# Kernel tuning notes

Hardware: AMD Instinct MI355X
Metric: run time of the kernel (lower is better)

## Reference

```python
import jax, jax.numpy as jnp
import numpy as np

N_ADDR, N_TX = 150000, 200000
IN_DIM, HID, HEADS = 64, 32, 4
DIM = HID // HEADS
E_AT, E_TA, E_AA = 1000000, 1000000, 500000
SLOPE = 0.2  # HANConv default negative_slope


def setup_inputs() -> dict:
    key = jax.random.key(0)
    ks = jax.random.split(key, 16)
    f = lambda k, shape, s: jax.random.normal(k, shape, dtype=jnp.float32) * s
    return {
        "x_addr": f(ks[0], (N_ADDR, IN_DIM), 1.0),
        "x_tx": f(ks[1], (N_TX, IN_DIM), 1.0),
        "e_at_src": jax.random.randint(ks[2], (E_AT,), 0, N_ADDR, dtype=jnp.int32),
        "e_at_dst": jax.random.randint(ks[3], (E_AT,), 0, N_TX, dtype=jnp.int32),
        "e_ta_src": jax.random.randint(ks[4], (E_TA,), 0, N_TX, dtype=jnp.int32),
        "e_ta_dst": jax.random.randint(ks[5], (E_TA,), 0, N_ADDR, dtype=jnp.int32),
        "e_aa_src": jax.random.randint(ks[6], (E_AA,), 0, N_ADDR, dtype=jnp.int32),
        "e_aa_dst": jax.random.randint(ks[7], (E_AA,), 0, N_ADDR, dtype=jnp.int32),
        "pW1": f(ks[8], (2, IN_DIM, HID), 0.1),      # layer-1 proj per node type [addr, tx]
        "pb1": jnp.zeros((2, HID), jnp.float32),
        "pW23": f(ks[9], (2, 2, HID, HID), 0.1),     # [layer-1, node_type]
        "pb23": jnp.zeros((2, 2, HID), jnp.float32),
        "att_src": f(ks[10], (3, 3, HEADS, DIM), 0.1),  # [layer, edge_type, H, D]
        "att_dst": f(ks[11], (3, 3, HEADS, DIM), 0.1),
        "kW": f(ks[12], (3, HID, HID), 0.1),         # semantic k_lin per layer
        "kb": jnp.zeros((3, HID), jnp.float32),
        "q": f(ks[13], (3, HID), 0.1),               # semantic query per layer
        "linW": f(ks[14], (HID, 2), 0.1),
        "linb": jnp.zeros((2,), jnp.float32),
    }


def _edge_softmax(logits, dst, n):
    # numerically stable segment softmax over destination neighborhoods
    m = jax.ops.segment_max(logits, dst, num_segments=n)          # [n, H]
    m = jnp.where(jnp.isfinite(m), m, 0.0)
    e = jnp.exp(logits - m[dst])
    s = jax.ops.segment_sum(e, dst, num_segments=n)
    return e / (s[dst] + 1e-16)


def _relation(h_src, h_dst, src, dst, a_s, a_d, n_dst):
    alpha_src = jnp.einsum('nhd,hd->nh', h_src, a_s)
    alpha_dst = jnp.einsum('nhd,hd->nh', h_dst, a_d)
    logit = alpha_src[src] + alpha_dst[dst]                        # [E, H]
    logit = jnp.where(logit >= 0, logit, SLOPE * logit)            # leaky_relu
    alpha = _edge_softmax(logit, dst, n_dst)
    msg = h_src[src] * alpha[:, :, None]                           # [E, H, D]
    out = jax.ops.segment_sum(msg, dst, num_segments=n_dst)        # [n_dst, H, D]
    return jax.nn.relu(out.reshape(n_dst, HID))


def _semantic(xs, kW, kb, q):
    # xs: [R, N, F]; semantic-level attention over R relations (PyG `group`)
    t = jnp.tanh(xs @ kW + kb).mean(axis=1)       # [R, F]
    attn = jax.nn.softmax((t * q).sum(-1))        # [R]
    return jnp.einsum('r,rnf->nf', attn, xs)


def _han_layer(x_a, x_t, Wa, ba, Wt, bt, a_s, a_d, kW, kb, q, edges):
    h_a = (x_a @ Wa + ba).reshape(-1, HEADS, DIM)
    h_t = (x_t @ Wt + bt).reshape(-1, HEADS, DIM)
    o_tx = _relation(h_a, h_t, edges[0], edges[1], a_s[0], a_d[0], N_TX)
    o_a1 = _relation(h_t, h_a, edges[2], edges[3], a_s[1], a_d[1], N_ADDR)
    o_a2 = _relation(h_a, h_a, edges[4], edges[5], a_s[2], a_d[2], N_ADDR)
    new_a = _semantic(jnp.stack([o_a1, o_a2]), kW, kb, q)
    new_t = _semantic(o_tx[None], kW, kb, q)
    return new_a, new_t


def reference(x_addr, x_tx, e_at_src, e_at_dst, e_ta_src, e_ta_dst,
              e_aa_src, e_aa_dst, pW1, pb1, pW23, pb23, att_src, att_dst,
              kW, kb, q, linW, linb):
    edges = (e_at_src, e_at_dst, e_ta_src, e_ta_dst, e_aa_src, e_aa_dst)
    a, t = _han_layer(x_addr, x_tx, pW1[0], pb1[0], pW1[1], pb1[1],
                      att_src[0], att_dst[0], kW[0], kb[0], q[0], edges)
    a, t = jax.nn.relu(a), jax.nn.relu(t)  # wrapper relu; dropout = eval identity
    for l in range(2):
        a, t = _han_layer(a, t, pW23[l, 0], pb23[l, 0], pW23[l, 1], pb23[l, 1],
                          att_src[l + 1], att_dst[l + 1],
                          kW[l + 1], kb[l + 1], q[l + 1], edges)
        a, t = jax.nn.relu(a), jax.nn.relu(t)
    return a @ linW + linb
```

## Files before the change

### kernel.cpp

```cpp
#include <hip/hip_runtime.h>
#include <hip/hip_bf16.h>
#include <hip/hip_fp16.h>

#define NA 150000
#define NT 200000
#define E_AT 1000000
#define E_TA 1000000
#define E_AA 500000

#define CHK 4096
#define CAP 8192
#define P_AT 391
#define P_TA 293
#define P_AA 293
#define NBINS (P_AT + P_TA + P_AA)
#define CB_AT 245
#define CB_TA 245
#define CB_AA 123
#define NBBIN (CB_AT + CB_TA + CB_AA)

#define GB_AT 6250
#define GB_TA 4688
#define GB_AA 4688

// ... 47 lines not shown
                       float* __restrict__ wts, int* __restrict__ flagp,
                       int* __restrict__ gcnt, float* __restrict__ sem) {
    __shared__ int cnt;
    const int t = threadIdx.x;
    if (t == 0) cnt = 0;
    __syncthreads();
    const unsigned short* u = (const unsigned short*)x;
    int wild = 0;
    for (int i = t; i < 4096; i += 256) {
        unsigned short v = u[i];
        int e = (v >> 7) & 0xFF;
        if (e > 133 || (e != 0 && e < 100)) wild++;
        else if (e == 0 && (v & 0x7F)) wild++;
    }
    atomicAdd(&cnt, wild);
    __syncthreads();
    const int f32 = (cnt > 1024) ? 1 : 0;
    if (t == 0) *flagp = f32;
    if (t < 8) sem[t] = 0.f;
    for (int i = t; i < 1024; i += 256) gcnt[i] = 0;
    for (int i = t; i < 4096; i += 256) wts[WO_W1 + i]  = ldf(pW1, i, f32);
    for (int i = t; i < 64;   i += 256) wts[WO_B1 + i]  = ldf(pb1, i, f32);
    for (int i = t; i < 4096; i += 256) wts[WO_W23 + i] = ldf(pW23, i, f32);
    for (int i = t; i < 128;  i += 256) wts[WO_B23 + i] = ldf(pb23, i, f32);
    for (int i = t; i < 288;  i += 256) wts[WO_AS + i]  = ldf(attS, i, f32);
    for (int i = t; i < 288;  i += 256) wts[WO_AD + i]  = ldf(attD, i, f32);
    for (int i = t; i < 3072; i += 256) wts[WO_KW + i]  = ldf(kW, i, f32);
    for (int i = t; i < 96;   i += 256) wts[WO_KB + i]  = ldf(kb, i, f32);
    for (int i = t; i < 96;   i += 256) wts[WO_Q + i]   = ldf(qv, i, f32);
    for (int i = t; i < 64;   i += 256) wts[WO_LW + i]  = ldf(linW, i, f32);
    for (int i = t; i < 2;    i += 256) wts[WO_LB + i]  = ldf(linb, i, f32);
}

__global__ __launch_bounds__(256) void k_projbin(
        const void* __restrict__ Xa, const void* __restrict__ Xt,
        const float* __restrict__ W, const float* __restrict__ Bv,
        unsigned short* __restrict__ Ha, unsigned short* __restrict__ Ht,
        const float* __restrict__ attD,
        float* __restrict__ ad0, float* __restrict__ ad1, float* __restrict__ ad2,
        const int* __restrict__ flagp,
        const int* __restrict__ eat_s, const int* __restrict__ eat_d,
        const int* __restrict__ eta_s, const int* __restrict__ eta_d,
        const int* __restrict__ eaa_s, const int* __restrict__ eaa_d,
        int* __restrict__ gcnt,
        int* __restrict__ slot_at, int* __restrict__ slot_ta, int* __restrict__ slot_aa) {
    __shared__ float smem[4224];
    const int t = threadIdx.x;
    int b = blockIdx.x;
    if (b < NBBIN) {
        int* hist = (int*)smem;
        const int *src, *dst; int E, P, seg; int* slot;
        if (b < CB_AT)              { src = eat_s; dst = eat_d; E = E_AT; P = P_AT; seg = 0;            slot = slot_at; }
        else if (b < CB_AT + CB_TA) { b -= CB_AT;  src = eta_s; dst = eta_d; E = E_TA; P = P_TA; seg = P_AT;        slot = slot_ta; }
        else                        { b -= CB_AT + CB_TA; src = eaa_s; dst = eaa_d; E = E_AA; P = P_AA; seg = P_AT + P_TA; slot = slot_aa; }
        long e0 = (long)b * CHK;
        for (int i = t; i < P; i += 256) hist[i] = 0;
        __syncthreads();
        for (int k = 0; k < CHK; k += 256) {
            long e = e0 + k + t;
            if (e < E) atomicAdd(&hist[dst[e] >> 9], 1);
        }
        __syncthreads();
        for (int i = t; i < P; i += 256) {
            int v = hist[i];
            hist[i] = atomicAdd(&gcnt[seg + i], v);
        }
        __syncthreads();
        for (int k = 0; k < CHK; k += 256) {
            long e = e0 + k + t;
            if (e < E) {
                int d = dst[e];
                int bin = d >> 9;
                int pos = atomicAdd(&hist[bin], 1);
                slot[bin * CAP + pos] = ((d & 511) << 18) | src[e];
            }
        }
        return;
    }
    b -= NBBIN;
    constexpr int K = 64, XS = K + 4, CPR = K / 4, TOT4 = 32 * CPR;
    float* Xs = smem;
    float* Wl = smem + 2176;
    const bool isA = b < GA32;
    const int bb = isA ? b : b - GA32;
    const int N = isA ? NA : NT;
    const int wOff = isA ? 0 : 2048;
    const int bOff = isA ? 0 : 32;
    const long n0 = (long)bb * 32;
    for (int i = t; i < K * 32; i += 256) Wl[i] = W[wOff + i];
    {
        const void* X = isA ? Xa : Xt;
        const int f32 = *flagp;
        if (f32) {
            const float* Xf = (const float*)X;
            for (int i = t; i < TOT4; i += 256) {
                int r = i / CPR, c = (i & (CPR - 1)) * 4;
                long gr = n0 + r; if (gr >= N) gr = N - 1;
                *(float4*)&Xs[r * XS + c] = *(const float4*)&Xf[gr * K + c];
            }
        } else {
            const unsigned short* Xh = (const unsigned short*)X;
            for (int i = t; i < TOT4; i += 256) {
                int r = i / CPR, c = (i & (CPR - 1)) * 4;
                long gr = n0 + r; if (gr >= N) gr = N - 1;
                ushort4 v = *(const ushort4*)&Xh[gr * K + c];
                float4 o;
                o.x = bf2f(v.x); o.y = bf2f(v.y); o.z = bf2f(v.z); o.w = bf2f(v.w);
                *(float4*)&Xs[r * XS + c] = o;
            }
        }
    }
    __syncthreads();
    const int g = t >> 3, q = t & 7;
    const long n = n0 + g;
    float a0 = Bv[bOff + q * 4 + 0];
    float a1 = Bv[bOff + q * 4 + 1];
    float a2 = Bv[bOff + q * 4 + 2];
    float a3 = Bv[bOff + q * 4 + 3];
#pragma unroll 4
    for (int k4 = 0; k4 < K; k4 += 4) {
        float4 xv = *(const float4*)&Xs[g * XS + k4];
        float4 w0 = *(const float4*)&Wl[(k4 + 0) * 32 + q * 4];
        float4 w1 = *(const float4*)&Wl[(k4 + 1) * 32 + q * 4];
        float4 w2 = *(const float4*)&Wl[(k4 + 2) * 32 + q * 4];
        float4 w3 = *(const float4*)&Wl[(k4 + 3) * 32 + q * 4];
        a0 = fmaf(xv.x, w0.x, a0); a1 = fmaf(xv.x, w0.y, a1);
        a2 = fmaf(xv.x, w0.z, a2); a3 = fmaf(xv.x, w0.w, a3);
        a0 = fmaf(xv.y, w1.x, a0); a1 = fmaf(xv.y, w1.y, a1);
        a2 = fmaf(xv.y, w1.z, a2); a3 = fmaf(xv.y, w1.w, a3);
        a0 = fmaf(xv.z, w2.x, a0); a1 = fmaf(xv.z, w2.y, a1);
        a2 = fmaf(xv.z, w2.z, a2); a3 = fmaf(xv.z, w2.w, a3);
        a0 = fmaf(xv.w, w3.x, a0); a1 = fmaf(xv.w, w3.y, a1);
        a2 = fmaf(xv.w, w3.z, a2); a3 = fmaf(xv.w, w3.w, a3);
    }
    if (n < N) {
        unsigned short* Hh = isA ? Ha : Ht;
        unsigned int p01 = (unsigned)f2h(a0) | ((unsigned)f2h(a1) << 16);
        unsigned int p23 = (unsigned)f2h(a2) | ((unsigned)f2h(a3) << 16);
        *(uint2*)&Hh[n * 32 + q * 4] = make_uint2(p01, p23);
        const int hh = q >> 1;
        const int ai = q * 4;
        if (isA) {
            float p1 = a0 * attD[ai + 32] + a1 * attD[ai + 33]
                     + a2 * attD[ai + 34] + a3 * attD[ai + 35];
            float p2 = a0 * attD[ai + 64] + a1 * attD[ai + 65]
                     + a2 * attD[ai + 66] + a3 * attD[ai + 67];
            float s1 = p1 + __shfl_xor(p1, 1);
            float s2 = p2 + __shfl_xor(p2, 1);
            if (!(q & 1)) { ad1[n * 4 + hh] = s1; ad2[n * 4 + hh] = s2; }
        } else {
            float p0 = a0 * attD[ai] + a1 * attD[ai + 1]
                     + a2 * attD[ai + 2] + a3 * attD[ai + 3];
            float s0 = p0 + __shfl_xor(p0, 1);
            if (!(q & 1)) ad0[n * 4 + hh] = s0;
        }
    }
}

__global__ __launch_bounds__(256) void k_proj2(
        const float* __restrict__ O1, const float* __restrict__ Ot,
        const float* __restrict__ O2, const float* __restrict__ semL,
        const float* __restrict__ W, int wOffA, int wOffT,
        const float* __restrict__ Bv, int bOffA, int bOffT,
        unsigned short* __restrict__ Ha, unsigned short* __restrict__ Ht,
        const float* __restrict__ attD, int lBase,
        float* __restrict__ ad0, float* __restrict__ ad1, float* __restrict__ ad2) {
    constexpr int K = 32, XS = K + 4, CPR = K / 4, TOT4 = 64 * CPR;
    __shared__ float Xs[64 * XS];
    __shared__ float Wl[K * 32];
    const int t = threadIdx.x;
    const bool isA = blockIdx.x < GA64;
    const int bb = isA ? (int)blockIdx.x : (int)blockIdx.x - GA64;
    const int N = isA ? NA : NT;
    const int wOff = isA ? wOffA : wOffT;
    const int bOff = isA ? bOffA : bOffT;
    const long n0 = (long)bb * 64;
    for (int i = t; i < K * 32; i += 256) Wl[i] = W[wOff + i];
    if (isA) {
        float s0 = semL[0] * (1.0f / NA), s1 = semL[1] * (1.0f / NA);
        float m = fmaxf(s0, s1);
        float e0 = __expf(s0 - m), e1 = __expf(s1 - m);
        float inv = 1.f / (e0 + e1);
        const float w0 = e0 * inv, w1 = e1 * inv;
        for (int i = t; i < TOT4; i += 256) {
            int r = i / CPR, c = (i & (CPR - 1)) * 4;
            long gr = n0 + r; if (gr >= N) gr = N - 1;
            float4 va = *(const float4*)&O1[gr * K + c];
            float4 vb = *(const float4*)&O2[gr * K + c];
            float4 o;
// ... 51 lines not shown
        if (isA) {
            float p1 = A0 * attD[ai + 32] + A1 * attD[ai + 33]
                     + A2 * attD[ai + 34] + A3 * attD[ai + 35];
            float p2 = A0 * attD[ai + 64] + A1 * attD[ai + 65]
                     + A2 * attD[ai + 66] + A3 * attD[ai + 67];
            float s1 = p1 + __shfl_xor(p1, 1);
            float s2 = p2 + __shfl_xor(p2, 1);
            if (!(q & 1)) { ad1[nA * 4 + hh] = s1; ad2[nA * 4 + hh] = s2; }
        } else {
            float p0 = A0 * attD[ai] + A1 * attD[ai + 1]
                     + A2 * attD[ai + 2] + A3 * attD[ai + 3];
            float s0 = p0 + __shfl_xor(p0, 1);
            if (!(q & 1)) ad0[nA * 4 + hh] = s0;
        }
    }
    if (nB < N) {
        unsigned int p01 = (unsigned)f2h(B0) | ((unsigned)f2h(B1) << 16);
        unsigned int p23 = (unsigned)f2h(B2) | ((unsigned)f2h(B3) << 16);
        *(uint2*)&Hh[nB * 32 + q * 4] = make_uint2(p01, p23);
        if (isA) {
            float p1 = B0 * attD[ai + 32] + B1 * attD[ai + 33]
                     + B2 * attD[ai + 34] + B3 * attD[ai + 35];
            float p2 = B0 * attD[ai + 64] + B1 * attD[ai + 65]
                     + B2 * attD[ai + 66] + B3 * attD[ai + 67];
            float s1 = p1 + __shfl_xor(p1, 1);
            float s2 = p2 + __shfl_xor(p2, 1);
            if (!(q & 1)) { ad1[nB * 4 + hh] = s1; ad2[nB * 4 + hh] = s2; }
        } else {
            float p0 = B0 * attD[ai] + B1 * attD[ai + 1]
                     + B2 * attD[ai + 2] + B3 * attD[ai + 3];
            float s0 = p0 + __shfl_xor(p0, 1);
            if (!(q & 1)) ad0[nB * 4 + hh] = s0;
        }
    }
}

__global__ __launch_bounds__(256) void k_binsort(
        const int* __restrict__ gcnt,
        const int* __restrict__ slot_at, const int* __restrict__ slot_ta,
        const int* __restrict__ slot_aa,
        int* __restrict__ off_at, int* __restrict__ off_ta, int* __restrict__ off_aa,
        int* __restrict__ csr_at, int* __restrict__ csr_ta, int* __restrict__ csr_aa) {
    __shared__ int sa[512], sb[512], cur[512];
    __shared__ int red[4];
    int b = blockIdx.x, t = threadIdx.x;
    const int* slot; int* off; int* csr; int N, bin, seg;
    if (b < P_AT)              { slot = slot_at; off = off_at; csr = csr_at; N = NT; bin = b;                seg = 0; }
    else if (b < P_AT + P_TA)  { slot = slot_ta; off = off_ta; csr = csr_ta; N = NA; bin = b - P_AT;         seg = P_AT; }
    else                       { slot = slot_aa; off = off_aa; csr = csr_aa; N = NA; bin = b - P_AT - P_TA;  seg = P_AT + P_TA; }
    if (b == 0 && t == 0) { off_at[NT] = E_AT; off_ta[NA] = E_TA; off_aa[NA] = E_AA; }
    int part = 0;
    for (int i = t; i < bin; i += 256) part += gcnt[seg + i];
    for (int o = 32; o > 0; o >>= 1) part += __shfl_xor(part, o, 64);
    if ((t & 63) == 0) red[t >> 6] = part;
    sa[t] = 0; sa[t + 256] = 0;
    __syncthreads();
    const int base = red[0] + red[1] + red[2] + red[3];
    const int cnt  = gcnt[seg + bin];
    const int* sp = &slot[bin * CAP];
    for (int i = t; i < cnt; i += 256) atomicAdd(&sa[sp[i] >> 18], 1);
    __syncthreads();
    int* in = sa; int* out = sb;
    for (int o = 1; o < 512; o <<= 1) {
        for (int i = t; i < 512; i += 256)
            out[i] = in[i] + (i >= o ? in[i - o] : 0);
        __syncthreads();
        int* tmp = in; in = out; out = tmp;
    }
    for (int i = t; i < 512; i += 256) {
        int excl = i ? in[i - 1] : 0;
        cur[i] = excl;
        int gd = bin * 512 + i;
        if (gd < N) off[gd] = base + excl;
    }
    __syncthreads();
    for (int i = t; i < cnt; i += 256) {
        int pk = sp[i];
        int pos = atomicAdd(&cur[pk >> 18], 1);
        csr[base + pos] = pk & 0x3FFFF;
    }
}

__global__ __launch_bounds__(256) void k_gather3(
        const int* __restrict__ off_at, const int* __restrict__ csr_at,
        const int* __restrict__ off_ta, const int* __restrict__ csr_ta,
        const int* __restrict__ off_aa, const int* __restrict__ csr_aa,
        const float* __restrict__ ad0, const float* __restrict__ ad1,
        const float* __restrict__ ad2,
        const unsigned short* __restrict__ h_a, const unsigned short* __restrict__ h_t,
        float* __restrict__ o_tx, float* __restrict__ o_a1, float* __restrict__ o_a2,
        const float* __restrict__ attS, int lBase, int gbAT) {
    int b = blockIdx.x;
    const int *off, *csr;
    const float *ad_;
    const unsigned short* Hs;
    float* O;
    int N, attOff;
    if (b < gbAT) {
        off = off_at; csr = csr_at; ad_ = ad0; Hs = h_a; O = o_tx; N = NT;
        attOff = lBase;
    } else if (b < gbAT + GB_TA) {
        b -= gbAT;
        off = off_ta; csr = csr_ta; ad_ = ad1; Hs = h_t; O = o_a1; N = NA;
        attOff = lBase + 32;
    } else {
        b -= gbAT + GB_TA;
        off = off_aa; csr = csr_aa; ad_ = ad2; Hs = h_a; O = o_a2; N = NA;
        attOff = lBase + 64;
    }
    const int t = threadIdx.x;
    const int q = t & 7;
    const int hh = q >> 1;
    const int n = b * 32 + (t >> 3);
    if (n >= N) return;
    const float4 aq = *(const float4*)&attS[attOff + q * 4];
    const float aq0 = aq.x, aq1 = aq.y, aq2 = aq.z, aq3 = aq.w;
    const float adv = ad_[n * 4 + hh];
    const int p0 = off[n], p1 = off[n + 1];
    float ax = 0.f, ay = 0.f, az = 0.f, aw = 0.f, se = 0.f;
    int p = p0;
    for (; p + 4 <= p1; p += 4) {
        int s0 = csr[p], s1 = csr[p + 1], s2 = csr[p + 2], s3 = csr[p + 3];
        ushort4 v0 = *(const ushort4*)&Hs[s0 * 32 + q * 4];
        ushort4 v1 = *(const ushort4*)&Hs[s1 * 32 + q * 4];
        ushort4 v2 = *(const ushort4*)&Hs[s2 * 32 + q * 4];
        ushort4 v3 = *(const ushort4*)&Hs[s3 * 32 + q * 4];
        float h00 = h2f(v0.x), h01 = h2f(v0.y), h02 = h2f(v0.z), h03 = h2f(v0.w);
        float h10 = h2f(v1.x), h11 = h2f(v1.y), h12 = h2f(v1.z), h13 = h2f(v1.w);
        float h20 = h2f(v2.x), h21 = h2f(v2.y), h22 = h2f(v2.z), h23 = h2f(v2.w);
        float h30 = h2f(v3.x), h31 = h2f(v3.y), h32 = h2f(v3.z), h33 = h2f(v3.w);
        float pt0 = h00 * aq0 + h01 * aq1 + h02 * aq2 + h03 * aq3;
        float pt1 = h10 * aq0 + h11 * aq1 + h12 * aq2 + h13 * aq3;
        float pt2 = h20 * aq0 + h21 * aq1 + h22 * aq2 + h23 * aq3;
        float pt3 = h30 * aq0 + h31 * aq1 + h32 * aq2 + h33 * aq3;
        float al0 = pt0 + __shfl_xor(pt0, 1);
        float al1 = pt1 + __shfl_xor(pt1, 1);
        float al2 = pt2 + __shfl_xor(pt2, 1);
        float al3 = pt3 + __shfl_xor(pt3, 1);
        float l0 = al0 + adv; l0 = fmaxf(l0, 0.2f * l0); float e0 = __expf(l0);
        float l1 = al1 + adv; l1 = fmaxf(l1, 0.2f * l1); float e1 = __expf(l1);
        float l2 = al2 + adv; l2 = fmaxf(l2, 0.2f * l2); float e2 = __expf(l2);
        float l3 = al3 + adv; l3 = fmaxf(l3, 0.2f * l3); float e3 = __expf(l3);
        se += e0 + e1 + e2 + e3;
        ax += e0 * h00 + e1 * h10 + e2 * h20 + e3 * h30;
        ay += e0 * h01 + e1 * h11 + e2 * h21 + e3 * h31;
        az += e0 * h02 + e1 * h12 + e2 * h22 + e3 * h32;
        aw += e0 * h03 + e1 * h13 + e2 * h23 + e3 * h33;
    }
    for (; p < p1; p++) {
        int s = csr[p];
        ushort4 v = *(const ushort4*)&Hs[s * 32 + q * 4];
        float h0 = h2f(v.x), h1 = h2f(v.y), h2 = h2f(v.z), h3 = h2f(v.w);
        float pt = h0 * aq0 + h1 * aq1 + h2 * aq2 + h3 * aq3;
        float al = pt + __shfl_xor(pt, 1);
        float l = al + adv; l = fmaxf(l, 0.2f * l);
        float e = __expf(l);
        se += e;
        ax += e * h0; ay += e * h1; az += e * h2; aw += e * h3;
    }
    const float inv = 1.f / (se + 1e-16f);
    float4 r;
    r.x = fmaxf(ax * inv, 0.f);
    r.y = fmaxf(ay * inv, 0.f);
    r.z = fmaxf(az * inv, 0.f);
    r.w = fmaxf(aw * inv, 0.f);
    *(float4*)&O[n * 32 + q * 4] = r;
}

__global__ __launch_bounds__(256) void k_sem_reduce(
        const float* __restrict__ O1, const float* __restrict__ O2,
        const float* __restrict__ kWl, const float* __restrict__ kbl,
        const float* __restrict__ qvl, float* __restrict__ semL) {
    __shared__ float w[1088];
    __shared__ float bacc;
    const int t = threadIdx.x;
    const int r = (blockIdx.x >= NB_SEM) ? 1 : 0;
    const float* O = r ? O2 : O1;
    for (int i = t; i < 1024; i += 256) w[i] = kWl[i];
    if (t < 32) w[1024 + t] = kbl[t];
    if (t >= 64 && t < 96) w[1056 + (t - 64)] = qvl[t - 64];
    if (t == 0) bacc = 0.f;
    __syncthreads();
    long n = (long)(blockIdx.x - r * NB_SEM) * 256 + t;
    float S = 0.f;
    if (n < NA) {
        float x[32];
#pragma unroll
        for (int k = 0; k < 32; k++) x[k] = O[n * 32 + k];
#pragma unroll
        for (int f = 0; f < 32; f++) {
            float acc = w[1024 + f];
#pragma unroll
            for (int k = 0; k < 32; k++) acc += x[k] * w[k * 32 + f];
            S += ftanh(acc) * w[1056 + f];
        }
    }
    for (int o = 32; o > 0; o >>= 1) S += __shfl_xor(S, o, 64);
    if ((t & 63) == 0) atomicAdd(&bacc, S);
    __syncthreads();
    if (t == 0) atomicAdd(&semL[r], bacc);
}

__global__ void k_combine_final(const float* __restrict__ o1, const float* __restrict__ o2,
                                const float* __restrict__ semL,
                                const float* __restrict__ linW, const float* __restrict__ linb,
                                void* __restrict__ out, int N, const int* __restrict__ flagp) {
    int n = blockIdx.x * blockDim.x + threadIdx.x;
    if (n >= N) return;
    int f32 = *flagp;
    float q0 = semL[0] * (1.0f / NA), q1 = semL[1] * (1.0f / NA);
    float m = fmaxf(q0, q1);
    float e0 = __expf(q0 - m), e1 = __expf(q1 - m);
    float ai = 1.f / (e0 + e1);
    float w0 = e0 * ai, w1 = e1 * ai;
    float s0 = linb[0], s1 = linb[1];
    const float* p1 = &o1[(long)n * 32];
// ... 39 lines not shown

    const size_t NA32 = (size_t)NA * 32, NT32 = (size_t)NT * 32;
    const size_t NA4 = (size_t)NA * 4, NT4 = (size_t)NT * 4;

    float* ws    = (float*)d_ws;
    float* h_aF  = ws;
    float* h_tF  = h_aF + NA32;
    float* o_a1  = h_tF + NT32;
    float* o_a2  = o_a1 + NA32;
    float* o_tx  = o_a2 + NA32;
    float* ad1   = o_tx + NT32;
    float* ad2   = ad1 + NA4;
    float* ad0   = ad2 + NA4;
    float* sem   = ad0 + NT4;
    int*   flagp = (int*)(sem + 8);
    int*   off_at = flagp + 16;
    int*   off_ta = off_at + (NT + 1);
    int*   off_aa = off_ta + (NA + 1);
    int*   csr_at = off_aa + (NA + 1);
    int*   csr_ta = csr_at + E_AT;
    int*   csr_aa = csr_ta + E_TA;
    int*   gcnt   = csr_aa + E_AA;
    int*   slot_at = gcnt + 1024;
    int*   slot_ta = slot_at + P_AT * CAP;
    int*   slot_aa = slot_ta + P_TA * CAP;
    float* wts    = (float*)(slot_aa + (size_t)P_AA * CAP);

    unsigned short* h_a = (unsigned short*)h_aF;
    unsigned short* h_t = (unsigned short*)h_tF;

    k_init<<<1, 256, 0, stream>>>(x_addr, pW1, pb1, pW23, pb23, attS, attD,
                                  kW, kb, qv, linW, linb, wts, flagp, gcnt, sem);

    k_projbin<<<NBBIN + GA32 + GT32, 256, 0, stream>>>(
        x_addr, x_tx, wts + WO_W1, wts + WO_B1, h_a, h_t, wts + WO_AD,
        ad0, ad1, ad2, flagp,
        eat_s, eat_d, eta_s, eta_d, eaa_s, eaa_d,
        gcnt, slot_at, slot_ta, slot_aa);
    k_binsort<<<NBINS, 256, 0, stream>>>(gcnt, slot_at, slot_ta, slot_aa,
                                         off_at, off_ta, off_aa, csr_at, csr_ta, csr_aa);

    for (int l = 0; l < 3; l++) {
        if (l > 0) {
            int wi = (l - 1) * 2;
            k_proj2<<<GA64 + GT64, 256, 0, stream>>>(
                o_a1, o_tx, o_a2, sem + 2 * (l - 1),
                wts + WO_W23, (wi + 0) * 1024, (wi + 1) * 1024,
                wts + WO_B23, (wi + 0) * 32, (wi + 1) * 32,
                h_a, h_t, wts + WO_AD, l * 96, ad0, ad1, ad2);
        }
        const int gbAT = (l < 2) ? GB_AT : 0;
        k_gather3<<<gbAT + GB_TA + GB_AA, 256, 0, stream>>>(
            off_at, csr_at, off_ta, csr_ta, off_aa, csr_aa,
            ad0, ad1, ad2, h_a, h_t, o_tx, o_a1, o_a2, wts + WO_AS, l * 96, gbAT);
        k_sem_reduce<<<2 * NB_SEM, 256, 0, stream>>>(
            o_a1, o_a2, wts + WO_KW + l * 1024, wts + WO_KB + l * 32,
            wts + WO_Q + l * 32, sem + 2 * l);
        if (l == 2) {
            k_combine_final<<<gblocks(NA), 256, 0, stream>>>(o_a1, o_a2, sem + 4,
                                                             wts + WO_LW, wts + WO_LB,
                                                             d_out, NA, flagp);
        }
    }
}
```

Measured before the change: 543.2 us.

## Rebalance kernel fusion to overlap tx projection with bin sort and AT gather with semantic reduce

Splits the combined projection/binning kernel so the tx-node projection runs alongside the CSR bin sort in one launch, and the address projection runs with edge binning. In each layer, the address-side gathers run first, and the tx-side gather is fused with the semantic-attention reduction, which depends only on the address outputs. The goal is to fill idle GPU capacity in small or tail-heavy kernels with independent work. The cost is heterogeneous blocks sharing one launch's resource limits, which may hurt occupancy or scheduling.

After: 573.8 us. +5.6%, slower.

```diff
diff --git a/kernel.cpp b/kernel.cpp
--- a/kernel.cpp
+++ b/kernel.cpp
@@ -103,10 +103,89 @@
     for (int i = t; i < 2;    i += 256) wts[WO_LB + i]  = ldf(linb, i, f32);
 }
 
-__global__ __launch_bounds__(256) void k_projbin(
-        const void* __restrict__ Xa, const void* __restrict__ Xt,
+__device__ __forceinline__ void proj1_body(
+        int bb, bool isA, const void* __restrict__ X, const float* __restrict__ W,
+        const float* __restrict__ Bv, unsigned short* __restrict__ Hh,
+        const float* __restrict__ attD,
+        float* __restrict__ ad0, float* __restrict__ ad1, float* __restrict__ ad2,
+        int f32, float* smem) {
+    constexpr int K = 64, XS = K + 4, CPR = K / 4, TOT4 = 32 * CPR;
+    const int t = threadIdx.x;
+    float* Xs = smem;
+    float* Wl = smem + 2176;
+    const int N = isA ? NA : NT;
+    const int wOff = isA ? 0 : 2048;
+    const int bOff = isA ? 0 : 32;
+    const long n0 = (long)bb * 32;
+    for (int i = t; i < K * 32; i += 256) Wl[i] = W[wOff + i];
+    if (f32) {
+        const float* Xf = (const float*)X;
+        for (int i = t; i < TOT4; i += 256) {
+            int r = i / CPR, c = (i & (CPR - 1)) * 4;
+            long gr = n0 + r; if (gr >= N) gr = N - 1;
+            *(float4*)&Xs[r * XS + c] = *(const float4*)&Xf[gr * K + c];
+        }
+    } else {
+        const unsigned short* Xh = (const unsigned short*)X;
+        for (int i = t; i < TOT4; i += 256) {
+            int r = i / CPR, c = (i & (CPR - 1)) * 4;
+            long gr = n0 + r; if (gr >= N) gr = N - 1;
+            ushort4 v = *(const ushort4*)&Xh[gr * K + c];
+            float4 o;
+            o.x = bf2f(v.x); o.y = bf2f(v.y); o.z = bf2f(v.z); o.w = bf2f(v.w);
+            *(float4*)&Xs[r * XS + c] = o;
+        }
+    }
+    __syncthreads();
+    const int g = t >> 3, q = t & 7;
+    const long n = n0 + g;
+    float a0 = Bv[bOff + q * 4 + 0];
+    float a1 = Bv[bOff + q * 4 + 1];
+    float a2 = Bv[bOff + q * 4 + 2];
+    float a3 = Bv[bOff + q * 4 + 3];
+#pragma unroll 4
+    for (int k4 = 0; k4 < K; k4 += 4) {
+        float4 xv = *(const float4*)&Xs[g * XS + k4];
+        float4 w0 = *(const float4*)&Wl[(k4 + 0) * 32 + q * 4];
+        float4 w1 = *(const float4*)&Wl[(k4 + 1) * 32 + q * 4];
+        float4 w2 = *(const float4*)&Wl[(k4 + 2) * 32 + q * 4];
+        float4 w3 = *(const float4*)&Wl[(k4 + 3) * 32 + q * 4];
+        a0 = fmaf(xv.x, w0.x, a0); a1 = fmaf(xv.x, w0.y, a1);
+        a2 = fmaf(xv.x, w0.z, a2); a3 = fmaf(xv.x, w0.w, a3);
+        a0 = fmaf(xv.y, w1.x, a0); a1 = fmaf(xv.y, w1.y, a1);
+        a2 = fmaf(xv.y, w1.z, a2); a3 = fmaf(xv.y, w1.w, a3);
+        a0 = fmaf(xv.z, w2.x, a0); a1 = fmaf(xv.z, w2.y, a1);
+        a2 = fmaf(xv.z, w2.z, a2); a3 = fmaf(xv.z, w2.w, a3);
+        a0 = fmaf(xv.w, w3.x, a0); a1 = fmaf(xv.w, w3.y, a1);
+        a2 = fmaf(xv.w, w3.z, a2); a3 = fmaf(xv.w, w3.w, a3);
+    }
+    if (n < N) {
+        unsigned int p01 = (unsigned)f2h(a0) | ((unsigned)f2h(a1) << 16);
+        unsigned int p23 = (unsigned)f2h(a2) | ((unsigned)f2h(a3) << 16);
+        *(uint2*)&Hh[n * 32 + q * 4] = make_uint2(p01, p23);
+        const int hh = q >> 1;
+        const int ai = q * 4;
+        if (isA) {
+            float p1 = a0 * attD[ai + 32] + a1 * attD[ai + 33]
+                     + a2 * attD[ai + 34] + a3 * attD[ai + 35];
+            float p2 = a0 * attD[ai + 64] + a1 * attD[ai + 65]
+                     + a2 * attD[ai + 66] + a3 * attD[ai + 67];
+            float s1 = p1 + __shfl_xor(p1, 1);
+            float s2 = p2 + __shfl_xor(p2, 1);
+            if (!(q & 1)) { ad1[n * 4 + hh] = s1; ad2[n * 4 + hh] = s2; }
+        } else {
+            float p0 = a0 * attD[ai] + a1 * attD[ai + 1]
+                     + a2 * attD[ai + 2] + a3 * attD[ai + 3];
+            float s0 = p0 + __shfl_xor(p0, 1);
+            if (!(q & 1)) ad0[n * 4 + hh] = s0;
+        }
+    }
+}
+
+__global__ __launch_bounds__(256) void k_binproja(
+        const void* __restrict__ Xa,
         const float* __restrict__ W, const float* __restrict__ Bv,
-        unsigned short* __restrict__ Ha, unsigned short* __restrict__ Ht,
+        unsigned short* __restrict__ Ha,
         const float* __restrict__ attD,
         float* __restrict__ ad0, float* __restrict__ ad1, float* __restrict__ ad2,
         const int* __restrict__ flagp,
@@ -148,84 +227,67 @@
         }
         return;
     }
-    b -= NBBIN;
-    constexpr int K = 64, XS = K + 4, CPR = K / 4, TOT4 = 32 * CPR;
-    float* Xs = smem;
-    float* Wl = smem + 2176;
-    const bool isA = b < GA32;
-    const int bb = isA ? b : b - GA32;
-    const int N = isA ? NA : NT;
-    const int wOff = isA ? 0 : 2048;
-    const int bOff = isA ? 0 : 32;
-    const long n0 = (long)bb * 32;
-    for (int i = t; i < K * 32; i += 256) Wl[i] = W[wOff + i];
-    {
-        const void* X = isA ? Xa : Xt;
-        const int f32 = *flagp;
-        if (f32) {
-            const float* Xf = (const float*)X;
-            for (int i = t; i < TOT4; i += 256) {
-                int r = i / CPR, c = (i & (CPR - 1)) * 4;
-                long gr = n0 + r; if (gr >= N) gr = N - 1;
-                *(float4*)&Xs[r * XS + c] = *(const float4*)&Xf[gr * K + c];
-            }
-        } else {
-            const unsigned short* Xh = (const unsigned short*)X;
-            for (int i = t; i < TOT4; i += 256) {
-                int r = i / CPR, c = (i & (CPR - 1)) * 4;
-                long gr = n0 + r; if (gr >= N) gr = N - 1;
-                ushort4 v = *(const ushort4*)&Xh[gr * K + c];
-                float4 o;
-                o.x = bf2f(v.x); o.y = bf2f(v.y); o.z = bf2f(v.z); o.w = bf2f(v.w);
-                *(float4*)&Xs[r * XS + c] = o;
-            }
-        }
-    }
-    __syncthreads();
-    const int g = t >> 3, q = t & 7;
-    const long n = n0 + g;
-    float a0 = Bv[bOff + q * 4 + 0];
-    float a1 = Bv[bOff + q * 4 + 1];
-    float a2 = Bv[bOff + q * 4 + 2];
-    float a3 = Bv[bOff + q * 4 + 3];
-#pragma unroll 4
-    for (int k4 = 0; k4 < K; k4 += 4) {
-        float4 xv = *(const float4*)&Xs[g * XS + k4];
-        float4 w0 = *(const float4*)&Wl[(k4 + 0) * 32 + q * 4];
-        float4 w1 = *(const float4*)&Wl[(k4 + 1) * 32 + q * 4];
-        float4 w2 = *(const float4*)&Wl[(k4 + 2) * 32 + q * 4];
-        float4 w3 = *(const float4*)&Wl[(k4 + 3) * 32 + q * 4];
-        a0 = fmaf(xv.x, w0.x, a0); a1 = fmaf(xv.x, w0.y, a1);
-        a2 = fmaf(xv.x, w0.z, a2); a3 = fmaf(xv.x, w0.w, a3);
-        a0 = fmaf(xv.y, w1.x, a0); a1 = fmaf(xv.y, w1.y, a1);
-        a2 = fmaf(xv.y, w1.z, a2); a3 = fmaf(xv.y, w1.w, a3);
-        a0 = fmaf(xv.z, w2.x, a0); a1 = fmaf(xv.z, w2.y, a1);
-        a2 = fmaf(xv.z, w2.z, a2); a3 = fmaf(xv.z, w2.w, a3);
-        a0 = fmaf(xv.w, w3.x, a0); a1 = fmaf(xv.w, w3.y, a1);
-        a2 = fmaf(xv.w, w3.z, a2); a3 = fmaf(xv.w, w3.w, a3);
-    }
-    if (n < N) {
-        unsigned short* Hh = isA ? Ha : Ht;
-        unsigned int p01 = (unsigned)f2h(a0) | ((unsigned)f2h(a1) << 16);
-        unsigned int p23 = (unsigned)f2h(a2) | ((unsigned)f2h(a3) << 16);
-        *(uint2*)&Hh[n * 32 + q * 4] = make_uint2(p01, p23);
-        const int hh = q >> 1;
-        const int ai = q * 4;
-        if (isA) {
-            float p1 = a0 * attD[ai + 32] + a1 * attD[ai + 33]
-                     + a2 * attD[ai + 34] + a3 * attD[ai + 35];
-            float p2 = a0 * attD[ai + 64] + a1 * attD[ai + 65]
-                     + a2 * attD[ai + 66] + a3 * attD[ai + 67];
-            float s1 = p1 + __shfl_xor(p1, 1);
-            float s2 = p2 + __shfl_xor(p2, 1);
-            if (!(q & 1)) { ad1[n * 4 + hh] = s1; ad2[n * 4 + hh] = s2; }
-        } else {
-            float p0 = a0 * attD[ai] + a1 * attD[ai + 1]
-                     + a2 * attD[ai + 2] + a3 * attD[ai + 3];
-            float s0 = p0 + __shfl_xor(p0, 1);
-            if (!(q & 1)) ad0[n * 4 + hh] = s0;
-        }
-    }
+    proj1_body(b - NBBIN, true, Xa, W, Bv, Ha, attD, ad0, ad1, ad2, *flagp, smem);
+}
+
+__global__ __launch_bounds__(256) void k_sortprojt(
+        const void* __restrict__ Xt,
+        const float* __restrict__ W, const float* __restrict__ Bv,
+        unsigned short* __restrict__ Ht,
+        const float* __restrict__ attD,
+        float* __restrict__ ad0, float* __restrict__ ad1, float* __restrict__ ad2,
+        const int* __restrict__ flagp,
+        const int* __restrict__ gcnt,
+        const int* __restrict__ slot_at, const int* __restrict__ slot_ta,
+        const int* __restrict__ slot_aa,
+        int* __restrict__ off_at, int* __restrict__ off_ta, int* __restrict__ off_aa,
+        int* __restrict__ csr_at, int* __restrict__ csr_ta, int* __restrict__ csr_aa) {
+    __shared__ float smem[4224];
+    const int t = threadIdx.x;
+    int b = blockIdx.x;
+    if (b < NBINS) {
+        int* sa  = (int*)smem;
+        int* sb  = sa + 512;
+        int* cur = sb + 512;
+        int* red = cur + 512;
+        const int* slot; int* off; int* csr; int N, bin, seg;
+        if (b < P_AT)              { slot = slot_at; off = off_at; csr = csr_at; N = NT; bin = b;                seg = 0; }
+        else if (b < P_AT + P_TA)  { slot = slot_ta; off = off_ta; csr = csr_ta; N = NA; bin = b - P_AT;         seg = P_AT; }
+        else                       { slot = slot_aa; off = off_aa; csr = csr_aa; N = NA; bin = b - P_AT - P_TA;  seg = P_AT + P_TA; }
+        if (b == 0 && t == 0) { off_at[NT] = E_AT; off_ta[NA] = E_TA; off_aa[NA] = E_AA; }
+        int part = 0;
+        for (int i = t; i < bin; i += 256) part += gcnt[seg + i];
+        for (int o = 32; o > 0; o >>= 1) part += __shfl_xor(part, o, 64);
+        if ((t & 63) == 0) red[t >> 6] = part;
+        sa[t] = 0; sa[t + 256] = 0;
+        __syncthreads();
+        const int base = red[0] + red[1] + red[2] + red[3];
+        const int cnt  = gcnt[seg + bin];
+        const int* sp = &slot[bin * CAP];
+        for (int i = t; i < cnt; i += 256) atomicAdd(&sa[sp[i] >> 18], 1);
+        __syncthreads();
+        int* in = sa; int* out = sb;
+        for (int o = 1; o < 512; o <<= 1) {
+            for (int i = t; i < 512; i += 256)
+                out[i] = in[i] + (i >= o ? in[i - o] : 0);
+            __syncthreads();
+            int* tmp = in; in = out; out = tmp;
+        }
+        for (int i = t; i < 512; i += 256) {
+            int excl = i ? in[i - 1] : 0;
+            cur[i] = excl;
+            int gd = bin * 512 + i;
+            if (gd < N) off[gd] = base + excl;
+        }
+        __syncthreads();
+        for (int i = t; i < cnt; i += 256) {
+            int pk = sp[i];
+            int pos = atomicAdd(&cur[pk >> 18], 1);
+            csr[base + pos] = pk & 0x3FFFF;
+        }
+        return;
+    }
+    proj1_body(b - NBINS, false, Xt, W, Bv, Ht, attD, ad0, ad1, ad2, *flagp, smem);
 }
 
 __global__ __launch_bounds__(256) void k_proj2(
@@ -346,79 +408,10 @@
     }
 }
 
-__global__ __launch_bounds__(256) void k_binsort(
-        const int* __restrict__ gcnt,
-        const int* __restrict__ slot_at, const int* __restrict__ slot_ta,
-        const int* __restrict__ slot_aa,
-        int* __restrict__ off_at, int* __restrict__ off_ta, int* __restrict__ off_aa,
-        int* __restrict__ csr_at, int* __restrict__ csr_ta, int* __restrict__ csr_aa) {
-    __shared__ int sa[512], sb[512], cur[512];
-    __shared__ int red[4];
-    int b = blockIdx.x, t = threadIdx.x;
-    const int* slot; int* off; int* csr; int N, bin, seg;
-    if (b < P_AT)              { slot = slot_at; off = off_at; csr = csr_at; N = NT; bin = b;                seg = 0; }
-    else if (b < P_AT + P_TA)  { slot = slot_ta; off = off_ta; csr = csr_ta; N = NA; bin = b - P_AT;         seg = P_AT; }
-    else                       { slot = slot_aa; off = off_aa; csr = csr_aa; N = NA; bin = b - P_AT - P_TA;  seg = P_AT + P_TA; }
-    if (b == 0 && t == 0) { off_at[NT] = E_AT; off_ta[NA] = E_TA; off_aa[NA] = E_AA; }
-    int part = 0;
-    for (int i = t; i < bin; i += 256) part += gcnt[seg + i];
-    for (int o = 32; o > 0; o >>= 1) part += __shfl_xor(part, o, 64);
-    if ((t & 63) == 0) red[t >> 6] = part;
-    sa[t] = 0; sa[t + 256] = 0;
-    __syncthreads();
-    const int base = red[0] + red[1] + red[2] + red[3];
-    const int cnt  = gcnt[seg + bin];
-    const int* sp = &slot[bin * CAP];
-    for (int i = t; i < cnt; i += 256) atomicAdd(&sa[sp[i] >> 18], 1);
-    __syncthreads();
-    int* in = sa; int* out = sb;
-    for (int o = 1; o < 512; o <<= 1) {
-        for (int i = t; i < 512; i += 256)
-            out[i] = in[i] + (i >= o ? in[i - o] : 0);
-        __syncthreads();
-        int* tmp = in; in = out; out = tmp;
-    }
-    for (int i = t; i < 512; i += 256) {
-        int excl = i ? in[i - 1] : 0;
-        cur[i] = excl;
-        int gd = bin * 512 + i;
-        if (gd < N) off[gd] = base + excl;
-    }
-    __syncthreads();
-    for (int i = t; i < cnt; i += 256) {
-        int pk = sp[i];
-        int pos = atomicAdd(&cur[pk >> 18], 1);
-        csr[base + pos] = pk & 0x3FFFF;
-    }
-}
-
-__global__ __launch_bounds__(256) void k_gather3(
-        const int* __restrict__ off_at, const int* __restrict__ csr_at,
-        const int* __restrict__ off_ta, const int* __restrict__ csr_ta,
-        const int* __restrict__ off_aa, const int* __restrict__ csr_aa,
-        const float* __restrict__ ad0, const float* __restrict__ ad1,
-        const float* __restrict__ ad2,
-        const unsigned short* __restrict__ h_a, const unsigned short* __restrict__ h_t,
-        float* __restrict__ o_tx, float* __restrict__ o_a1, float* __restrict__ o_a2,
-        const float* __restrict__ attS, int lBase, int gbAT) {
-    int b = blockIdx.x;
-    const int *off, *csr;
-    const float *ad_;
-    const unsigned short* Hs;
-    float* O;
-    int N, attOff;
-    if (b < gbAT) {
-        off = off_at; csr = csr_at; ad_ = ad0; Hs = h_a; O = o_tx; N = NT;
-        attOff = lBase;
-    } else if (b < gbAT + GB_TA) {
-        b -= gbAT;
-        off = off_ta; csr = csr_ta; ad_ = ad1; Hs = h_t; O = o_a1; N = NA;
-        attOff = lBase + 32;
-    } else {
-        b -= gbAT + GB_TA;
-        off = off_aa; csr = csr_aa; ad_ = ad2; Hs = h_a; O = o_a2; N = NA;
-        attOff = lBase + 64;
-    }
+__device__ __forceinline__ void gather_body(
+        int b, const int* __restrict__ off, const int* __restrict__ csr,
+        const float* __restrict__ ad_, const unsigned short* __restrict__ Hs,
+        float* __restrict__ O, int N, const float* __restrict__ attS, int attOff) {
     const int t = threadIdx.x;
     const int q = t & 7;
     const int hh = q >> 1;
@@ -478,21 +471,46 @@
     *(float4*)&O[n * 32 + q * 4] = r;
 }
 
-__global__ __launch_bounds__(256) void k_sem_reduce(
+__global__ __launch_bounds__(256) void k_gather_a(
+        const int* __restrict__ off_ta, const int* __restrict__ csr_ta,
+        const int* __restrict__ off_aa, const int* __restrict__ csr_aa,
+        const float* __restrict__ ad1, const float* __restrict__ ad2,
+        const unsigned short* __restrict__ h_a, const unsigned short* __restrict__ h_t,
+        float* __restrict__ o_a1, float* __restrict__ o_a2,
+        const float* __restrict__ attS, int lBase) {
+    int b = blockIdx.x;
+    if (b < GB_TA)
+        gather_body(b, off_ta, csr_ta, ad1, h_t, o_a1, NA, attS, lBase + 32);
+    else
+        gather_body(b - GB_TA, off_aa, csr_aa, ad2, h_a, o_a2, NA, attS, lBase + 64);
+}
+
+__global__ __launch_bounds__(256) void k_gatsem(
+        const int* __restrict__ off_at, const int* __restrict__ csr_at,
+        const float* __restrict__ ad0,
+        const unsigned short* __restrict__ h_a,
+        float* __restrict__ o_tx,
+        const float* __restrict__ attS, int lBase, int gbAT,
         const float* __restrict__ O1, const float* __restrict__ O2,
         const float* __restrict__ kWl, const float* __restrict__ kbl,
         const float* __restrict__ qvl, float* __restrict__ semL) {
     __shared__ float w[1088];
     __shared__ float bacc;
+    int b = blockIdx.x;
+    if (b < gbAT) {
+        gather_body(b, off_at, csr_at, ad0, h_a, o_tx, NT, attS, lBase);
+        return;
+    }
+    b -= gbAT;
     const int t = threadIdx.x;
-    const int r = (blockIdx.x >= NB_SEM) ? 1 : 0;
+    const int r = (b >= NB_SEM) ? 1 : 0;
     const float* O = r ? O2 : O1;
     for (int i = t; i < 1024; i += 256) w[i] = kWl[i];
     if (t < 32) w[1024 + t] = kbl[t];
     if (t >= 64 && t < 96) w[1056 + (t - 64)] = qvl[t - 64];
     if (t == 0) bacc = 0.f;
     __syncthreads();
-    long n = (long)(blockIdx.x - r * NB_SEM) * 256 + t;
+    long n = (long)(b - r * NB_SEM) * 256 + t;
     float S = 0.f;
     if (n < NA) {
         float x[32];
@@ -598,13 +616,16 @@
     k_init<<<1, 256, 0, stream>>>(x_addr, pW1, pb1, pW23, pb23, attS, attD,
                                   kW, kb, qv, linW, linb, wts, flagp, gcnt, sem);
 
-    k_projbin<<<NBBIN + GA32 + GT32, 256, 0, stream>>>(
-        x_addr, x_tx, wts + WO_W1, wts + WO_B1, h_a, h_t, wts + WO_AD,
+    k_binproja<<<NBBIN + GA32, 256, 0, stream>>>(
+        x_addr, wts + WO_W1, wts + WO_B1, h_a, wts + WO_AD,
         ad0, ad1, ad2, flagp,
         eat_s, eat_d, eta_s, eta_d, eaa_s, eaa_d,
         gcnt, slot_at, slot_ta, slot_aa);
-    k_binsort<<<NBINS, 256, 0, stream>>>(gcnt, slot_at, slot_ta, slot_aa,
-                                         off_at, off_ta, off_aa, csr_at, csr_ta, csr_aa);
+    k_sortprojt<<<NBINS + GT32, 256, 0, stream>>>(
+        x_tx, wts + WO_W1, wts + WO_B1, h_t, wts + WO_AD,
+        ad0, ad1, ad2, flagp,
+        gcnt, slot_at, slot_ta, slot_aa,
+        off_at, off_ta, off_aa, csr_at, csr_ta, csr_aa);
 
     for (int l = 0; l < 3; l++) {
         if (l > 0) {
@@ -615,11 +636,12 @@
                 wts + WO_B23, (wi + 0) * 32, (wi + 1) * 32,
                 h_a, h_t, wts + WO_AD, l * 96, ad0, ad1, ad2);
         }
+        k_gather_a<<<GB_TA + GB_AA, 256, 0, stream>>>(
+            off_ta, csr_ta, off_aa, csr_aa, ad1, ad2, h_a, h_t,
+            o_a1, o_a2, wts + WO_AS, l * 96);
         const int gbAT = (l < 2) ? GB_AT : 0;
-        k_gather3<<<gbAT + GB_TA + GB_AA, 256, 0, stream>>>(
-            off_at, csr_at, off_ta, csr_ta, off_aa, csr_aa,
-            ad0, ad1, ad2, h_a, h_t, o_tx, o_a1, o_a2, wts + WO_AS, l * 96, gbAT);
-        k_sem_reduce<<<2 * NB_SEM, 256, 0, stream>>>(
+        k_gatsem<<<gbAT + 2 * NB_SEM, 256, 0, stream>>>(
+            off_at, csr_at, ad0, h_a, o_tx, wts + WO_AS, l * 96, gbAT,
             o_a1, o_a2, wts + WO_KW + l * 1024, wts + WO_KB + l * 32,
             wts + WO_Q + l * 32, sem + 2 * l);
         if (l == 2) {
```

## Split layer-1 projection so tx projection overlaps with CSR bin sort

Applied to the files above, without the earlier changes.

Moves the tx-node projection out of the binning+projection kernel and merges it into the bin-sort kernel, so the sort blocks (few, latency-bound) share a launch with the tx projection blocks. The projection body becomes a shared device function. The aim is to balance work across the two kernels and fill idle CUs during the sort. Shared memory is sized for the larger of the two roles, and the sort blocks now allocate more LDS than before, which may reduce occupancy.

New measurement: 547.3 us. No clear change (+0.7%).

```diff
diff --git a/kernel.cpp b/kernel.cpp
--- a/kernel.cpp
+++ b/kernel.cpp
@@ -103,10 +103,89 @@
     for (int i = t; i < 2;    i += 256) wts[WO_LB + i]  = ldf(linb, i, f32);
 }
 
-__global__ __launch_bounds__(256) void k_projbin(
-        const void* __restrict__ Xa, const void* __restrict__ Xt,
+__device__ __forceinline__ void proj1_body(
+        int bb, bool isA, const void* __restrict__ X, const float* __restrict__ W,
+        const float* __restrict__ Bv, unsigned short* __restrict__ Hh,
+        const float* __restrict__ attD,
+        float* __restrict__ ad0, float* __restrict__ ad1, float* __restrict__ ad2,
+        int f32, float* smem) {
+    constexpr int K = 64, XS = K + 4, CPR = K / 4, TOT4 = 32 * CPR;
+    const int t = threadIdx.x;
+    float* Xs = smem;
+    float* Wl = smem + 2176;
+    const int N = isA ? NA : NT;
+    const int wOff = isA ? 0 : 2048;
+    const int bOff = isA ? 0 : 32;
+    const long n0 = (long)bb * 32;
+    for (int i = t; i < K * 32; i += 256) Wl[i] = W[wOff + i];
+    if (f32) {
+        const float* Xf = (const float*)X;
+        for (int i = t; i < TOT4; i += 256) {
+            int r = i / CPR, c = (i & (CPR - 1)) * 4;
+            long gr = n0 + r; if (gr >= N) gr = N - 1;
+            *(float4*)&Xs[r * XS + c] = *(const float4*)&Xf[gr * K + c];
+        }
+    } else {
+        const unsigned short* Xh = (const unsigned short*)X;
+        for (int i = t; i < TOT4; i += 256) {
+            int r = i / CPR, c = (i & (CPR - 1)) * 4;
+            long gr = n0 + r; if (gr >= N) gr = N - 1;
+            ushort4 v = *(const ushort4*)&Xh[gr * K + c];
+            float4 o;
+            o.x = bf2f(v.x); o.y = bf2f(v.y); o.z = bf2f(v.z); o.w = bf2f(v.w);
+            *(float4*)&Xs[r * XS + c] = o;
+        }
+    }
+    __syncthreads();
+    const int g = t >> 3, q = t & 7;
+    const long n = n0 + g;
+    float a0 = Bv[bOff + q * 4 + 0];
+    float a1 = Bv[bOff + q * 4 + 1];
+    float a2 = Bv[bOff + q * 4 + 2];
+    float a3 = Bv[bOff + q * 4 + 3];
+#pragma unroll 4
+    for (int k4 = 0; k4 < K; k4 += 4) {
+        float4 xv = *(const float4*)&Xs[g * XS + k4];
+        float4 w0 = *(const float4*)&Wl[(k4 + 0) * 32 + q * 4];
+        float4 w1 = *(const float4*)&Wl[(k4 + 1) * 32 + q * 4];
+        float4 w2 = *(const float4*)&Wl[(k4 + 2) * 32 + q * 4];
+        float4 w3 = *(const float4*)&Wl[(k4 + 3) * 32 + q * 4];
+        a0 = fmaf(xv.x, w0.x, a0); a1 = fmaf(xv.x, w0.y, a1);
+        a2 = fmaf(xv.x, w0.z, a2); a3 = fmaf(xv.x, w0.w, a3);
+        a0 = fmaf(xv.y, w1.x, a0); a1 = fmaf(xv.y, w1.y, a1);
+        a2 = fmaf(xv.y, w1.z, a2); a3 = fmaf(xv.y, w1.w, a3);
+        a0 = fmaf(xv.z, w2.x, a0); a1 = fmaf(xv.z, w2.y, a1);
+        a2 = fmaf(xv.z, w2.z, a2); a3 = fmaf(xv.z, w2.w, a3);
+        a0 = fmaf(xv.w, w3.x, a0); a1 = fmaf(xv.w, w3.y, a1);
+        a2 = fmaf(xv.w, w3.z, a2); a3 = fmaf(xv.w, w3.w, a3);
+    }
+    if (n < N) {
+        unsigned int p01 = (unsigned)f2h(a0) | ((unsigned)f2h(a1) << 16);
+        unsigned int p23 = (unsigned)f2h(a2) | ((unsigned)f2h(a3) << 16);
+        *(uint2*)&Hh[n * 32 + q * 4] = make_uint2(p01, p23);
+        const int hh = q >> 1;
+        const int ai = q * 4;
+        if (isA) {
+            float p1 = a0 * attD[ai + 32] + a1 * attD[ai + 33]
+                     + a2 * attD[ai + 34] + a3 * attD[ai + 35];
+            float p2 = a0 * attD[ai + 64] + a1 * attD[ai + 65]
+                     + a2 * attD[ai + 66] + a3 * attD[ai + 67];
+            float s1 = p1 + __shfl_xor(p1, 1);
+            float s2 = p2 + __shfl_xor(p2, 1);
+            if (!(q & 1)) { ad1[n * 4 + hh] = s1; ad2[n * 4 + hh] = s2; }
+        } else {
+            float p0 = a0 * attD[ai] + a1 * attD[ai + 1]
+                     + a2 * attD[ai + 2] + a3 * attD[ai + 3];
+            float s0 = p0 + __shfl_xor(p0, 1);
+            if (!(q & 1)) ad0[n * 4 + hh] = s0;
+        }
+    }
+}
+
+__global__ __launch_bounds__(256) void k_binproja(
+        const void* __restrict__ Xa,
         const float* __restrict__ W, const float* __restrict__ Bv,
-        unsigned short* __restrict__ Ha, unsigned short* __restrict__ Ht,
+        unsigned short* __restrict__ Ha,
         const float* __restrict__ attD,
         float* __restrict__ ad0, float* __restrict__ ad1, float* __restrict__ ad2,
         const int* __restrict__ flagp,
@@ -148,84 +227,67 @@
         }
         return;
     }
-    b -= NBBIN;
-    constexpr int K = 64, XS = K + 4, CPR = K / 4, TOT4 = 32 * CPR;
-    float* Xs = smem;
-    float* Wl = smem + 2176;
-    const bool isA = b < GA32;
-    const int bb = isA ? b : b - GA32;
-    const int N = isA ? NA : NT;
-    const int wOff = isA ? 0 : 2048;
-    const int bOff = isA ? 0 : 32;
-    const long n0 = (long)bb * 32;
-    for (int i = t; i < K * 32; i += 256) Wl[i] = W[wOff + i];
-    {
-        const void* X = isA ? Xa : Xt;
-        const int f32 = *flagp;
-        if (f32) {
-            const float* Xf = (const float*)X;
-            for (int i = t; i < TOT4; i += 256) {
-                int r = i / CPR, c = (i & (CPR - 1)) * 4;
-                long gr = n0 + r; if (gr >= N) gr = N - 1;
-                *(float4*)&Xs[r * XS + c] = *(const float4*)&Xf[gr * K + c];
-            }
-        } else {
-            const unsigned short* Xh = (const unsigned short*)X;
-            for (int i = t; i < TOT4; i += 256) {
-                int r = i / CPR, c = (i & (CPR - 1)) * 4;
-                long gr = n0 + r; if (gr >= N) gr = N - 1;
-                ushort4 v = *(const ushort4*)&Xh[gr * K + c];
-                float4 o;
-                o.x = bf2f(v.x); o.y = bf2f(v.y); o.z = bf2f(v.z); o.w = bf2f(v.w);
-                *(float4*)&Xs[r * XS + c] = o;
-            }
-        }
-    }
-    __syncthreads();
-    const int g = t >> 3, q = t & 7;
-    const long n = n0 + g;
-    float a0 = Bv[bOff + q * 4 + 0];
-    float a1 = Bv[bOff + q * 4 + 1];
-    float a2 = Bv[bOff + q * 4 + 2];
-    float a3 = Bv[bOff + q * 4 + 3];
-#pragma unroll 4
-    for (int k4 = 0; k4 < K; k4 += 4) {
-        float4 xv = *(const float4*)&Xs[g * XS + k4];
-        float4 w0 = *(const float4*)&Wl[(k4 + 0) * 32 + q * 4];
-        float4 w1 = *(const float4*)&Wl[(k4 + 1) * 32 + q * 4];
-        float4 w2 = *(const float4*)&Wl[(k4 + 2) * 32 + q * 4];
-        float4 w3 = *(const float4*)&Wl[(k4 + 3) * 32 + q * 4];
-        a0 = fmaf(xv.x, w0.x, a0); a1 = fmaf(xv.x, w0.y, a1);
-        a2 = fmaf(xv.x, w0.z, a2); a3 = fmaf(xv.x, w0.w, a3);
-        a0 = fmaf(xv.y, w1.x, a0); a1 = fmaf(xv.y, w1.y, a1);
-        a2 = fmaf(xv.y, w1.z, a2); a3 = fmaf(xv.y, w1.w, a3);
-        a0 = fmaf(xv.z, w2.x, a0); a1 = fmaf(xv.z, w2.y, a1);
-        a2 = fmaf(xv.z, w2.z, a2); a3 = fmaf(xv.z, w2.w, a3);
-        a0 = fmaf(xv.w, w3.x, a0); a1 = fmaf(xv.w, w3.y, a1);
-        a2 = fmaf(xv.w, w3.z, a2); a3 = fmaf(xv.w, w3.w, a3);
-    }
-    if (n < N) {
-        unsigned short* Hh = isA ? Ha : Ht;
-        unsigned int p01 = (unsigned)f2h(a0) | ((unsigned)f2h(a1) << 16);
-        unsigned int p23 = (unsigned)f2h(a2) | ((unsigned)f2h(a3) << 16);
-        *(uint2*)&Hh[n * 32 + q * 4] = make_uint2(p01, p23);
-        const int hh = q >> 1;
-        const int ai = q * 4;
-        if (isA) {
-            float p1 = a0 * attD[ai + 32] + a1 * attD[ai + 33]
-                     + a2 * attD[ai + 34] + a3 * attD[ai + 35];
-            float p2 = a0 * attD[ai + 64] + a1 * attD[ai + 65]
-                     + a2 * attD[ai + 66] + a3 * attD[ai + 67];
-            float s1 = p1 + __shfl_xor(p1, 1);
-            float s2 = p2 + __shfl_xor(p2, 1);
-            if (!(q & 1)) { ad1[n * 4 + hh] = s1; ad2[n * 4 + hh] = s2; }
-        } else {
-            float p0 = a0 * attD[ai] + a1 * attD[ai + 1]
-                     + a2 * attD[ai + 2] + a3 * attD[ai + 3];
-            float s0 = p0 + __shfl_xor(p0, 1);
-            if (!(q & 1)) ad0[n * 4 + hh] = s0;
-        }
-    }
+    proj1_body(b - NBBIN, true, Xa, W, Bv, Ha, attD, ad0, ad1, ad2, *flagp, smem);
+}
+
+__global__ __launch_bounds__(256) void k_sortprojt(
+        const void* __restrict__ Xt,
+        const float* __restrict__ W, const float* __restrict__ Bv,
+        unsigned short* __restrict__ Ht,
+        const float* __restrict__ attD,
+        float* __restrict__ ad0, float* __restrict__ ad1, float* __restrict__ ad2,
+        const int* __restrict__ flagp,
+        const int* __restrict__ gcnt,
+        const int* __restrict__ slot_at, const int* __restrict__ slot_ta,
+        const int* __restrict__ slot_aa,
+        int* __restrict__ off_at, int* __restrict__ off_ta, int* __restrict__ off_aa,
+        int* __restrict__ csr_at, int* __restrict__ csr_ta, int* __restrict__ csr_aa) {
+    __shared__ float smem[4224];
+    const int t = threadIdx.x;
+    int b = blockIdx.x;
+    if (b < NBINS) {
+        int* sa  = (int*)smem;
+        int* sb  = sa + 512;
+        int* cur = sb + 512;
+        int* red = cur + 512;
+        const int* slot; int* off; int* csr; int N, bin, seg;
+        if (b < P_AT)              { slot = slot_at; off = off_at; csr = csr_at; N = NT; bin = b;                seg = 0; }
+        else if (b < P_AT + P_TA)  { slot = slot_ta; off = off_ta; csr = csr_ta; N = NA; bin = b - P_AT;         seg = P_AT; }
+        else                       { slot = slot_aa; off = off_aa; csr = csr_aa; N = NA; bin = b - P_AT - P_TA;  seg = P_AT + P_TA; }
+        if (b == 0 && t == 0) { off_at[NT] = E_AT; off_ta[NA] = E_TA; off_aa[NA] = E_AA; }
+        int part = 0;
+        for (int i = t; i < bin; i += 256) part += gcnt[seg + i];
+        for (int o = 32; o > 0; o >>= 1) part += __shfl_xor(part, o, 64);
+        if ((t & 63) == 0) red[t >> 6] = part;
+        sa[t] = 0; sa[t + 256] = 0;
+        __syncthreads();
+        const int base = red[0] + red[1] + red[2] + red[3];
+        const int cnt  = gcnt[seg + bin];
+        const int* sp = &slot[bin * CAP];
+        for (int i = t; i < cnt; i += 256) atomicAdd(&sa[sp[i] >> 18], 1);
+        __syncthreads();
+        int* in = sa; int* out = sb;
+        for (int o = 1; o < 512; o <<= 1) {
+            for (int i = t; i < 512; i += 256)
+                out[i] = in[i] + (i >= o ? in[i - o] : 0);
+            __syncthreads();
+            int* tmp = in; in = out; out = tmp;
+        }
+        for (int i = t; i < 512; i += 256) {
+            int excl = i ? in[i - 1] : 0;
+            cur[i] = excl;
+            int gd = bin * 512 + i;
+            if (gd < N) off[gd] = base + excl;
+        }
+        __syncthreads();
+        for (int i = t; i < cnt; i += 256) {
+            int pk = sp[i];
+            int pos = atomicAdd(&cur[pk >> 18], 1);
+            csr[base + pos] = pk & 0x3FFFF;
+        }
+        return;
+    }
+    proj1_body(b - NBINS, false, Xt, W, Bv, Ht, attD, ad0, ad1, ad2, *flagp, smem);
 }
 
 __global__ __launch_bounds__(256) void k_proj2(
@@ -343,52 +405,6 @@
             float s0 = p0 + __shfl_xor(p0, 1);
             if (!(q & 1)) ad0[nB * 4 + hh] = s0;
         }
-    }
-}
-
-__global__ __launch_bounds__(256) void k_binsort(
-        const int* __restrict__ gcnt,
-        const int* __restrict__ slot_at, const int* __restrict__ slot_ta,
-        const int* __restrict__ slot_aa,
-        int* __restrict__ off_at, int* __restrict__ off_ta, int* __restrict__ off_aa,
-        int* __restrict__ csr_at, int* __restrict__ csr_ta, int* __restrict__ csr_aa) {
-    __shared__ int sa[512], sb[512], cur[512];
-    __shared__ int red[4];
-    int b = blockIdx.x, t = threadIdx.x;
-    const int* slot; int* off; int* csr; int N, bin, seg;
-    if (b < P_AT)              { slot = slot_at; off = off_at; csr = csr_at; N = NT; bin = b;                seg = 0; }
-    else if (b < P_AT + P_TA)  { slot = slot_ta; off = off_ta; csr = csr_ta; N = NA; bin = b - P_AT;         seg = P_AT; }
-    else                       { slot = slot_aa; off = off_aa; csr = csr_aa; N = NA; bin = b - P_AT - P_TA;  seg = P_AT + P_TA; }
-    if (b == 0 && t == 0) { off_at[NT] = E_AT; off_ta[NA] = E_TA; off_aa[NA] = E_AA; }
-    int part = 0;
-    for (int i = t; i < bin; i += 256) part += gcnt[seg + i];
-    for (int o = 32; o > 0; o >>= 1) part += __shfl_xor(part, o, 64);
-    if ((t & 63) == 0) red[t >> 6] = part;
-    sa[t] = 0; sa[t + 256] = 0;
-    __syncthreads();
-    const int base = red[0] + red[1] + red[2] + red[3];
-    const int cnt  = gcnt[seg + bin];
-    const int* sp = &slot[bin * CAP];
-    for (int i = t; i < cnt; i += 256) atomicAdd(&sa[sp[i] >> 18], 1);
-    __syncthreads();
-    int* in = sa; int* out = sb;
-    for (int o = 1; o < 512; o <<= 1) {
-        for (int i = t; i < 512; i += 256)
-            out[i] = in[i] + (i >= o ? in[i - o] : 0);
-        __syncthreads();
-        int* tmp = in; in = out; out = tmp;
-    }
-    for (int i = t; i < 512; i += 256) {
-        int excl = i ? in[i - 1] : 0;
-        cur[i] = excl;
-        int gd = bin * 512 + i;
-        if (gd < N) off[gd] = base + excl;
-    }
-    __syncthreads();
-    for (int i = t; i < cnt; i += 256) {
-        int pk = sp[i];
-        int pos = atomicAdd(&cur[pk >> 18], 1);
-        csr[base + pos] = pk & 0x3FFFF;
     }
 }
 
@@ -598,13 +614,16 @@
     k_init<<<1, 256, 0, stream>>>(x_addr, pW1, pb1, pW23, pb23, attS, attD,
                                   kW, kb, qv, linW, linb, wts, flagp, gcnt, sem);
 
-    k_projbin<<<NBBIN + GA32 + GT32, 256, 0, stream>>>(
-        x_addr, x_tx, wts + WO_W1, wts + WO_B1, h_a, h_t, wts + WO_AD,
+    k_binproja<<<NBBIN + GA32, 256, 0, stream>>>(
+        x_addr, wts + WO_W1, wts + WO_B1, h_a, wts + WO_AD,
         ad0, ad1, ad2, flagp,
         eat_s, eat_d, eta_s, eta_d, eaa_s, eaa_d,
         gcnt, slot_at, slot_ta, slot_aa);
-    k_binsort<<<NBINS, 256, 0, stream>>>(gcnt, slot_at, slot_ta, slot_aa,
-                                         off_at, off_ta, off_aa, csr_at, csr_ta, csr_aa);
+    k_sortprojt<<<NBINS + GT32, 256, 0, stream>>>(
+        x_tx, wts + WO_W1, wts + WO_B1, h_t, wts + WO_AD,
+        ad0, ad1, ad2, flagp,
+        gcnt, slot_at, slot_ta, slot_aa,
+        off_at, off_ta, off_aa, csr_at, csr_ta, csr_aa);
 
     for (int l = 0; l < 3; l++) {
         if (l > 0) {
```
